# Kernel optimization log

Hardware: AMD Instinct MI355X
Metric: run time of the kernel (lower is better)

## Reference

```python
import jax, jax.numpy as jnp
import numpy as np

N, E = 20000, 320000
IN, HID, R, HEADS = 128, 256, 4, 4
C = HID // HEADS  # per-head dim


def setup_inputs() -> dict:
    key = jax.random.key(0)
    ks = jax.random.split(key, 20)
    g = lambda k, s, sc=0.05: jax.random.normal(k, s, jnp.float32) * sc
    return {
        'x': g(ks[0], (N, IN), 1.0),
        'edge_index': jax.random.randint(ks[1], (2, E), 0, N),
        'edge_type': jax.random.randint(ks[2], (E,), 0, R),
        'h_prev': g(ks[3], (N, HID), 1.0),
        # RGCN layer 1: relation weights, root weight, bias
        'W1': g(ks[4], (R, IN, HID)), 'root1': g(ks[5], (IN, HID)), 'b1': jnp.zeros((HID,), jnp.float32),
        # RGCN layer 2
        'W2': g(ks[6], (R, HID, HID)), 'root2': g(ks[7], (HID, HID)), 'b2': jnp.zeros((HID,), jnp.float32),
        # TransformerConv linears (query/key/value/skip), each Linear(HID, HEADS*C)
        'Wq': g(ks[8], (HID, HID)), 'bq': jnp.zeros((HID,), jnp.float32),
        'Wk': g(ks[9], (HID, HID)), 'bk': jnp.zeros((HID,), jnp.float32),
        'Wv': g(ks[10], (HID, HID)), 'bv': jnp.zeros((HID,), jnp.float32),
        'Wskip': g(ks[11], (HID, HID)), 'bskip': jnp.zeros((HID,), jnp.float32),
        # GRUCell (torch layout: [3*HID, in], gates ordered r, z, n)
        'W_ih': g(ks[12], (3 * HID, HID)), 'b_ih': jnp.zeros((3 * HID,), jnp.float32),
        'W_hh': g(ks[13], (3 * HID, HID)), 'b_hh': jnp.zeros((3 * HID,), jnp.float32),
    }


def rgcn(x, src, dst, etype, W, Wroot, b):
    # PyG RGCNConv: out_i = x_i @ Wroot + b + sum_r mean_{j in N_r(i)} x_j @ W_r
    n = x.shape[0]
    out = x @ Wroot + b
    xs = x[src]  # [E, F_in]
    for r in range(W.shape[0]):  # small fixed relation count
        mask = (etype == r).astype(x.dtype)  # [E]
        msg = (xs @ W[r]) * mask[:, None]  # [E, F_out]
        agg = jax.ops.segment_sum(msg, dst, num_segments=n)
        cnt = jax.ops.segment_sum(mask, dst, num_segments=n)
        out = out + agg / jnp.maximum(cnt, 1.0)[:, None]
    return out


def transformer_conv(x, src, dst, Wq, bq, Wk, bk, Wv, bv, Wskip, bskip):
    # PyG TransformerConv, concat=True, root_weight=True
    n = x.shape[0]
    q = (x @ Wq + bq).reshape(n, HEADS, C)
    k = (x @ Wk + bk).reshape(n, HEADS, C)
    v = (x @ Wv + bv).reshape(n, HEADS, C)
    score = jnp.einsum('ehc,ehc->eh', q[dst], k[src]) * (1.0 / np.sqrt(C))  # [E, H]
    smax = jax.ops.segment_max(score, dst, num_segments=n)  # [N, H]
    ex = jnp.exp(score - smax[dst])
    denom = jax.ops.segment_sum(ex, dst, num_segments=n)
    alpha = ex / jnp.maximum(denom[dst], 1e-16)  # edge softmax per dst node
    out = jax.ops.segment_sum(alpha[:, :, None] * v[src], dst, num_segments=n)  # [N, H, C]
    return out.reshape(n, HEADS * C) + x @ Wskip + bskip


def gru_cell(xi, h, W_ih, b_ih, W_hh, b_hh):
    gi = xi @ W_ih.T + b_ih
    gh = h @ W_hh.T + b_hh
    ir, iz, inn = jnp.split(gi, 3, axis=1)
    hr, hz, hn = jnp.split(gh, 3, axis=1)
    r = jax.nn.sigmoid(ir + hr)
    z = jax.nn.sigmoid(iz + hz)
    nw = jnp.tanh(inn + r * hn)
    return (1.0 - z) * nw + z * h


def reference(x, edge_index, edge_type, h_prev, W1, root1, b1, W2, root2, b2,
              Wq, bq, Wk, bk, Wv, bv, Wskip, bskip, W_ih, b_ih, W_hh, b_hh):
    src, dst = edge_index[0], edge_index[1]
    h = jax.nn.relu(rgcn(x, src, dst, edge_type, W1, root1, b1))
    h = jax.nn.relu(rgcn(h, src, dst, edge_type, W2, root2, b2))
    h = transformer_conv(h, src, dst, Wq, bq, Wk, bk, Wv, bv, Wskip, bskip)
    h = gru_cell(h, h_prev, W_ih, b_ih, W_hh, b_hh)
    return h
```

## Files before the change

kernel.cpp:

```cpp
#include <hip/hip_runtime.h>
#include <hip/hip_bf16.h>
#include <stdint.h>

#define N_NODES 20000
#define E_EDGES 320000
#define IN_F    128
#define HIDF    256
#define R_REL   4
#define NRKEYS  (N_NODES*R_REL)
#define SCAN_BLOCKS 80

typedef __attribute__((ext_vector_type(8))) short  short8;
typedef __attribute__((ext_vector_type(4))) float  floatx4;

__device__ __forceinline__ float bf2f(__hip_bfloat16 v){ return __bfloat162float(v); }
__device__ __forceinline__ __hip_bfloat16 f2bf(float v){ return __float2bfloat16(v); }
__device__ __forceinline__ float bfbits2f(unsigned short u){ return __uint_as_float(((unsigned)u)<<16); }
__device__ __forceinline__ unsigned short f2bfbits(float v){
    __hip_bfloat16 h = __float2bfloat16(v);
    return *(unsigned short*)&h;
}
__device__ __forceinline__ unsigned pack_bf2(float a, float b){
    return (unsigned)f2bfbits(a) | ((unsigned)f2bfbits(b) << 16);
}

__device__ __forceinline__ void gload_lds16(const void* g, void* l)
{
    __builtin_amdgcn_global_load_lds((const __attribute__((address_space(1))) void*)g,
                                     (__attribute__((address_space(3))) void*)l, 16, 0, 0);
}

template<int N>
__device__ __forceinline__ void wait_vm()
{
    if constexpr (N == 0)      asm volatile("s_waitcnt vmcnt(0)" ::: "memory");
    else if constexpr (N == 3) asm volatile("s_waitcnt vmcnt(3)" ::: "memory");
    else if constexpr (N == 4) asm volatile("s_waitcnt vmcnt(4)" ::: "memory");
    else                       asm volatile("s_waitcnt vmcnt(0)" ::: "memory");
}

__device__ __forceinline__ int2 xcd_swizzle()
{
    int gx = gridDim.x, gy = gridDim.y;
    int nwg = gx * gy;
    int lin = blockIdx.x + gx * blockIdx.y;
    int q = nwg >> 3, r = nwg & 7;
    int k = lin & 7, i = lin >> 3;
    int j = (k < r ? k*(q+1) : r*(q+1) + (k-r)*q) + i;
    return make_int2(j / gy, j % gy);
}

__global__ void count_kernel(const int* __restrict__ ei, const int* __restrict__ et,
                             int* __restrict__ cnt)
{
    int e = blockIdx.x*256 + threadIdx.x;
    if (e >= E_EDGES) return;
    int dst = ei[E_EDGES + e];
    atomicAdd(&cnt[dst*R_REL + et[e]], 1);
}

__global__ __launch_bounds__(1024) void scan_reduce_kernel(const int* __restrict__ cnt,
                                                           int* __restrict__ blocksum)
{
    int ix = blockIdx.x*1024 + threadIdx.x;
    int v = (ix < NRKEYS) ? cnt[ix] : 0;
    #pragma unroll
    for (int o=32;o>0;o>>=1) v += __shfl_xor(v, o, 64);
    __shared__ int wsum[16];
    int wave = threadIdx.x >> 6, lane = threadIdx.x & 63;
    if (lane == 0) wsum[wave] = v;
    __syncthreads();
    if (threadIdx.x == 0) {
        int s = 0;
        #pragma unroll
        for (int w=0;w<16;w++) s += wsum[w];
        blocksum[blockIdx.x] = s;
    }
}

__global__ __launch_bounds__(128) void scan_sums_kernel(const int* __restrict__ blocksum,
                                                        int* __restrict__ blockoff)
{
    __shared__ int s[128];
    int t = threadIdx.x;
    int v = (t < SCAN_BLOCKS) ? blocksum[t] : 0;
    s[t] = v; __syncthreads();
    for (int off=1; off<128; off<<=1) {
        int u = (t>=off) ? s[t-off] : 0;
        __syncthreads();
        s[t] += u;
        __syncthreads();
    }
    if (t < SCAN_BLOCKS) blockoff[t] = s[t] - v;
}

__global__ __launch_bounds__(1024) void scan_apply_kernel(const int* __restrict__ cnt,
                                                          const int* __restrict__ blockoff,
                                                          int* __restrict__ row_ptr,
                                                          int* __restrict__ cursor)
{
    __shared__ int s[1024];
    int t = threadIdx.x;
    int ix = blockIdx.x*1024 + t;
    int v = (ix < NRKEYS) ? cnt[ix] : 0;
    s[t] = v; __syncthreads();
    for (int off=1; off<1024; off<<=1) {
        int u = (t>=off) ? s[t-off] : 0;
        __syncthreads();
        s[t] += u;
        __syncthreads();
    }
    if (ix < NRKEYS) {
        int excl = blockoff[blockIdx.x] + s[t] - v;
        row_ptr[ix] = excl;
        cursor[ix]  = excl;
        if (ix == NRKEYS-1) row_ptr[NRKEYS] = excl + v;
    }
}

__global__ void fill_kernel(const int* __restrict__ ei, const int* __restrict__ et,
                            int* __restrict__ cursor, int* __restrict__ csr_src)
{
    int e = blockIdx.x*256 + threadIdx.x;
    if (e >= E_EDGES) return;
    int src = ei[e];
    int dst = ei[E_EDGES + e];
    int key = dst*R_REL + et[e];
    int pos = atomicAdd(&cursor[key], 1);
    csr_src[pos] = src;
}

__global__ void make_b1t(const float* __restrict__ root1,
                         const float* __restrict__ W1,
                         __hip_bfloat16* __restrict__ B1t)
{
    int idx = blockIdx.x*256 + threadIdx.x;
    if (idx >= 256*640) return;
    int n = idx / 640, k = idx % 640;
    float v;
    if (k < 128) v = root1[k*256 + n];
    else         v = W1[(k-128)*256 + n];
    B1t[idx] = f2bf(v);
}

__global__ void make_b2t(const float* __restrict__ root2,
                         const float* __restrict__ W2,
                         __hip_bfloat16* __restrict__ B2t)
{
    int idx = blockIdx.x*256 + threadIdx.x;
    if (idx >= 256*1280) return;
    int n = idx / 1280, k = idx % 1280;
    float v;
    if (k < 256) v = root2[k*256 + n];
    else         v = W2[(k-256)*256 + n];
    B2t[idx] = f2bf(v);
}

__global__ void make_b3t(const float* __restrict__ Wq, const float* __restrict__ Wk,
                         const float* __restrict__ Wv, const float* __restrict__ Wsk,
                         const float* __restrict__ bq, const float* __restrict__ bk,
                         const float* __restrict__ bv, const float* __restrict__ bsk,
                         __hip_bfloat16* __restrict__ B3t, float* __restrict__ bias3)
{
    int idx = blockIdx.x*256 + threadIdx.x;
    if (idx >= 1024*256) return;
    int n = idx / 256, k = idx % 256;
    int g = n >> 8, nn = n & 255;
    const float* W = (g==0)?Wq:(g==1)?Wk:(g==2)?Wv:Wsk;
    B3t[idx] = f2bf(W[k*256 + nn]);
    if (k == 0) {
        const float* B = (g==0)?bq:(g==1)?bk:(g==2)?bv:bsk;
        bias3[n] = B[nn];
    }
}

__global__ void cvt_f32_bf16(const float* __restrict__ in, __hip_bfloat16* __restrict__ out, int n)
{
    int i = blockIdx.x*256 + threadIdx.x;
    if (i < n) out[i] = f2bf(in[i]);
}

__global__ __launch_bounds__(256) void agg1_kernel(const float* __restrict__ x,
                                                   const int* __restrict__ row_ptr,
                                                   const int* __restrict__ csr_src,
                                                   __hip_bfloat16* __restrict__ A1)
{
    int b = blockIdx.x*4 + (threadIdx.x >> 6);
    int lane = threadIdx.x & 63;
    int i = b >> 2, r = b & 3;
    int e0 = row_ptr[b], e1 = row_ptr[b+1];
    float sx0=0.f,sy0=0.f, sx1=0.f,sy1=0.f, sx2=0.f,sy2=0.f, sx3=0.f,sy3=0.f;
    int e = e0;
    for (; e+4 <= e1; e += 4) {
        int i0=csr_src[e], i1=csr_src[e+1], i2=csr_src[e+2], i3=csr_src[e+3];
        float2 v0 = *(const float2*)(x + (size_t)i0*IN_F + lane*2);
        float2 v1 = *(const float2*)(x + (size_t)i1*IN_F + lane*2);
        float2 v2 = *(const float2*)(x + (size_t)i2*IN_F + lane*2);
        float2 v3 = *(const float2*)(x + (size_t)i3*IN_F + lane*2);
        sx0+=v0.x; sy0+=v0.y; sx1+=v1.x; sy1+=v1.y;
        sx2+=v2.x; sy2+=v2.y; sx3+=v3.x; sy3+=v3.y;
    }
    for (; e < e1; e++) {
        int i0 = csr_src[e];
        float2 v = *(const float2*)(x + (size_t)i0*IN_F + lane*2);
        sx0+=v.x; sy0+=v.y;
    }
    float sx = (sx0+sx1)+(sx2+sx3);
    float sy = (sy0+sy1)+(sy2+sy3);
    float inv = (e1>e0) ? 1.f/(float)(e1-e0) : 0.f;
    *(unsigned*)(A1 + (size_t)i*640 + 128 + r*128 + lane*2) = pack_bf2(sx*inv, sy*inv);
    if (r == 0) {
        float2 v = *(const float2*)(x + (size_t)i*IN_F + lane*2);
        *(unsigned*)(A1 + (size_t)i*640 + lane*2) = pack_bf2(v.x, v.y);
    }
}

__global__ __launch_bounds__(256) void agg2_kernel(const int* __restrict__ row_ptr,
                                                   const int* __restrict__ csr_src,
                                                   __hip_bfloat16* __restrict__ A2)
{
    int b = blockIdx.x*4 + (threadIdx.x >> 6);
    int lane = threadIdx.x & 63;
    int i = b >> 2, r = b & 3;
    int e0 = row_ptr[b], e1 = row_ptr[b+1];
    float a0=0.f,a1=0.f,a2=0.f,a3=0.f;
    float b0=0.f,b1=0.f,b2=0.f,b3=0.f;
    float c0=0.f,c1=0.f,c2=0.f,c3=0.f;
    float d0=0.f,d1=0.f,d2=0.f,d3=0.f;
    int e = e0;
    for (; e+4 <= e1; e += 4) {
        int i0=csr_src[e], i1=csr_src[e+1], i2=csr_src[e+2], i3=csr_src[e+3];
        ushort4 u0 = *(const ushort4*)(A2 + (size_t)i0*1280 + lane*4);
        ushort4 u1 = *(const ushort4*)(A2 + (size_t)i1*1280 + lane*4);
        ushort4 u2 = *(const ushort4*)(A2 + (size_t)i2*1280 + lane*4);
        ushort4 u3 = *(const ushort4*)(A2 + (size_t)i3*1280 + lane*4);
        a0+=bfbits2f(u0.x); a1+=bfbits2f(u0.y); a2+=bfbits2f(u0.z); a3+=bfbits2f(u0.w);
        b0+=bfbits2f(u1.x); b1+=bfbits2f(u1.y); b2+=bfbits2f(u1.z); b3+=bfbits2f(u1.w);
        c0+=bfbits2f(u2.x); c1+=bfbits2f(u2.y); c2+=bfbits2f(u2.z); c3+=bfbits2f(u2.w);
        d0+=bfbits2f(u3.x); d1+=bfbits2f(u3.y); d2+=bfbits2f(u3.z); d3+=bfbits2f(u3.w);
    }
    for (; e < e1; e++) {
        int i0 = csr_src[e];
        ushort4 u = *(const ushort4*)(A2 + (size_t)i0*1280 + lane*4);
        a0+=bfbits2f(u.x); a1+=bfbits2f(u.y); a2+=bfbits2f(u.z); a3+=bfbits2f(u.w);
    }
    float s0=(a0+b0)+(c0+d0), s1=(a1+b1)+(c1+d1), s2=(a2+b2)+(c2+d2), s3=(a3+b3)+(c3+d3);
    float inv = (e1>e0) ? 1.f/(float)(e1-e0) : 0.f;
    uint2 w;
    w.x = pack_bf2(s0*inv, s1*inv);
    w.y = pack_bf2(s2*inv, s3*inv);
    *(uint2*)(A2 + (size_t)i*1280 + 256 + r*256 + lane*4) = w;
}

template<int MI>
__device__ __forceinline__ void gemm_bt_body(const __hip_bfloat16* __restrict__ A, int lda,
                                             const __hip_bfloat16* __restrict__ Bt,
                                             const float* __restrict__ bias,
                                             __hip_bfloat16* __restrict__ C, int ldc,
                                             int M, int K, int relu,
                                             int tile_m, int tile_n,
                                             __hip_bfloat16* lds_a, __hip_bfloat16* lds_b)
{
    constexpr int A_ELEMS = MI*1024;
    constexpr int B_ELEMS = 4096;
    constexpr int L = MI/2 + 2;
    const int tid  = threadIdx.x;
    const int wave = tid >> 6;
    const int lane = tid & 63;
    const int wm = wave >> 1, wn = wave & 1;
    const int fm = lane & 15;
    const int q  = lane >> 4;
    const int sw = (q ^ ((fm >> 1) & 3)) * 8;

    floatx4 acc[MI][4];
    #pragma unroll
    for (int i=0;i<MI;i++)
        #pragma unroll
        for (int j=0;j<4;j++) acc[i][j] = (floatx4){0.f,0.f,0.f,0.f};

    const int srow   = lane >> 2;
    const int schunk = lane & 3;
    size_t a_goff[MI/2];
    #pragma unroll
    for (int s = 0; s < MI/2; ++s) {
        int r = (s*4 + wave)*16 + srow;
        int c = schunk ^ ((r >> 1) & 3);
        a_goff[s] = (size_t)min(tile_m + r, M-1)*lda + c*8;
    }
    size_t b_goff[2];
    #pragma unroll
    for (int s = 0; s < 2; ++s) {
        int r = (s*4 + wave)*16 + srow;
        int c = schunk ^ ((r >> 1) & 3);
        b_goff[s] = (size_t)(tile_n + r)*K + c*8;
    }

    const int nt = K >> 5;

    auto issue = [&](int t, int bufi) {
        const int kn = t << 5;
        #pragma unroll
        for (int s = 0; s < MI/2; ++s)
            gload_lds16(A + a_goff[s] + kn, lds_a + bufi*A_ELEMS + (s*4 + wave)*512);
        #pragma unroll
        for (int s = 0; s < 2; ++s)
            gload_lds16(Bt + b_goff[s] + kn, lds_b + bufi*B_ELEMS + (s*4 + wave)*512);
    };

    issue(0, 0);
    if (nt > 1) { issue(1, 1); wait_vm<L>(); }
    else        { wait_vm<0>(); }
    __builtin_amdgcn_s_barrier();

    int cur = 0, nx2 = 2;
    for (int t = 0; t < nt; ++t) {
        if (t + 2 < nt) issue(t + 2, nx2);

        const __hip_bfloat16* la = lds_a + cur*A_ELEMS;
        const __hip_bfloat16* lb = lds_b + cur*B_ELEMS;
        short8 afr[MI], bfr[4];
        #pragma unroll
        for (int i=0;i<MI;i++)
            afr[i] = *(const short8*)(la + (wm*(MI*16) + i*16 + fm)*32 + sw);
        #pragma unroll
        for (int j=0;j<4;j++)
            bfr[j] = *(const short8*)(lb + (wn*64 + j*16 + fm)*32 + sw);

        __builtin_amdgcn_s_setprio(1);
        #pragma unroll
        for (int i=0;i<MI;i++)
            #pragma unroll
            for (int j=0;j<4;j++)
                acc[i][j] = __builtin_amdgcn_mfma_f32_16x16x32_bf16(afr[i], bfr[j], acc[i][j], 0,0,0);
        __builtin_amdgcn_s_setprio(0);

        if (t + 1 < nt) {
            if (t + 2 < nt) wait_vm<L>();
            else            wait_vm<0>();
            __builtin_amdgcn_s_barrier();
            cur = (cur == 2) ? 0 : cur + 1;
            nx2 = (nx2 == 2) ? 0 : nx2 + 1;
        }
    }

    const int crow_base = tile_m + wm*(MI*16);
    const int ccol_base = tile_n + wn*64;
    #pragma unroll
    for (int i=0;i<MI;i++) {
        #pragma unroll
        for (int j=0;j<4;j++) {
            int c  = ccol_base + j*16 + fm;
            float bb = bias[c];
            #pragma unroll
            for (int rg=0; rg<4; rg++) {
                int r = crow_base + i*16 + q*4 + rg;
                if (r < M) {
                    float v = acc[i][j][rg] + bb;
                    if (relu) v = fmaxf(v, 0.f);
                    C[(size_t)r*ldc + c] = f2bf(v);
                }
            }
        }
    }
}

template<int MI>
__global__ __launch_bounds__(256) void gemm_bt_t(const __hip_bfloat16* __restrict__ A, int lda,
                                                 const __hip_bfloat16* __restrict__ Bt,
                                                 const float* __restrict__ bias,
                                                 __hip_bfloat16* __restrict__ C, int ldc,
                                                 int M, int K, int relu)
{
    __shared__ __align__(16) __hip_bfloat16 lds_a[3*MI*1024];
    __shared__ __align__(16) __hip_bfloat16 lds_b[3*4096];
    int2 xy = xcd_swizzle();
    gemm_bt_body<MI>(A, lda, Bt, bias, C, ldc, M, K, relu,
                     xy.x*(MI*32), xy.y*128, lds_a, lds_b);
}

__global__ __launch_bounds__(256) void gemm_bt_dual(const __hip_bfloat16* __restrict__ A0,
                                                    const __hip_bfloat16* __restrict__ A1,
                                                    const __hip_bfloat16* __restrict__ Bt0,
                                                    const __hip_bfloat16* __restrict__ Bt1,
                                                    const float* __restrict__ bias0,
                                                    const float* __restrict__ bias1,
                                                    __hip_bfloat16* __restrict__ C0,
                                                    __hip_bfloat16* __restrict__ C1)
{
    __shared__ __align__(16) __hip_bfloat16 lds_a[3*4096];
    __shared__ __align__(16) __hip_bfloat16 lds_b[3*4096];
    int2 xy = xcd_swizzle();
    int which = xy.y >= 6;
    int ty    = which ? (xy.y - 6) : xy.y;
    gemm_bt_body<4>(which ? A1 : A0, 256,
                    which ? Bt1 : Bt0,
                    which ? bias1 : bias0,
                    which ? C1 : C0, 768,
                    N_NODES, 256, 0,
                    xy.x*128, ty*128, lds_a, lds_b);
}

__global__ __launch_bounds__(256) void score_kernel(const __hip_bfloat16* __restrict__ qkvs,
                                                    const int* __restrict__ row_ptr,
                                                    const int* __restrict__ csr_src,
                                                    float* __restrict__ score)
{
    int i = blockIdx.x*4 + (threadIdx.x >> 6);
    int lane = threadIdx.x & 63;
    int h = lane >> 4, d4 = lane & 15;
    int e0 = row_ptr[i*R_REL], e1 = row_ptr[i*R_REL + R_REL];
    ushort4 qv = *(const ushort4*)(qkvs + (size_t)i*1024 + lane*4);
    float qx=bfbits2f(qv.x), qy=bfbits2f(qv.y), qz=bfbits2f(qv.z), qw=bfbits2f(qv.w);
    float* sp = score + (size_t)h*E_EDGES;
    int j = e0;
    for (; j+2 <= e1; j += 2) {
        int s0 = csr_src[j], s1 = csr_src[j+1];
        ushort4 k0 = *(const ushort4*)(qkvs + (size_t)s0*1024 + 256 + lane*4);
        ushort4 k1 = *(const ushort4*)(qkvs + (size_t)s1*1024 + 256 + lane*4);
        float d0 = qx*bfbits2f(k0.x)+qy*bfbits2f(k0.y)+qz*bfbits2f(k0.z)+qw*bfbits2f(k0.w);
        float d1 = qx*bfbits2f(k1.x)+qy*bfbits2f(k1.y)+qz*bfbits2f(k1.z)+qw*bfbits2f(k1.w);
        #pragma unroll
        for (int o=1;o<16;o<<=1){ d0 += __shfl_xor(d0,o,64); d1 += __shfl_xor(d1,o,64); }
        if (d4 == 0) { sp[j] = d0*0.125f; sp[j+1] = d1*0.125f; }
    }
    for (; j < e1; j++) {
        int s0 = csr_src[j];
        ushort4 k0 = *(const ushort4*)(qkvs + (size_t)s0*1024 + 256 + lane*4);
        float d0 = qx*bfbits2f(k0.x)+qy*bfbits2f(k0.y)+qz*bfbits2f(k0.z)+qw*bfbits2f(k0.w);
        #pragma unroll
        for (int o=1;o<16;o<<=1) d0 += __shfl_xor(d0,o,64);
        if (d4 == 0) sp[j] = d0*0.125f;
    }
}

__global__ __launch_bounds__(256) void attn_agg_kernel(const __hip_bfloat16* __restrict__ qkvs,
                                                       const float* __restrict__ score,
                                                       const int* __restrict__ row_ptr,
                                                       const int* __restrict__ csr_src,
                                                       __hip_bfloat16* __restrict__ hatt)
{
    int i = blockIdx.x*4 + (threadIdx.x >> 6);
    int lane = threadIdx.x & 63;
    int h  = lane >> 4;
    int d4 = lane & 15;
    int e0 = row_ptr[i*R_REL], e1 = row_ptr[i*R_REL + R_REL];
    int deg = e1 - e0;
    const float* sp = score + (size_t)h*E_EDGES + e0;

    float m = -1e30f;
    for (int j = d4; j < deg; j += 16) m = fmaxf(m, sp[j]);
    #pragma unroll
    for (int o=1;o<16;o<<=1) m = fmaxf(m, __shfl_xor(m, o, 64));

    float ssum = 0.f;
    for (int j = d4; j < deg; j += 16) ssum += __expf(sp[j] - m);
    #pragma unroll
    for (int o=1;o<16;o<<=1) ssum += __shfl_xor(ssum, o, 64);
    float inv = 1.f / fmaxf(ssum, 1e-16f);

    float ax=0.f, ay=0.f, az=0.f, aw=0.f;
    int j = 0;
    for (; j+4 <= deg; j += 4) {
        int s0=csr_src[e0+j], s1=csr_src[e0+j+1], s2=csr_src[e0+j+2], s3=csr_src[e0+j+3];
        float w0 = __expf(sp[j]   - m) * inv;
        float w1 = __expf(sp[j+1] - m) * inv;
        float w2 = __expf(sp[j+2] - m) * inv;
        float w3 = __expf(sp[j+3] - m) * inv;
        ushort4 u0 = *(const ushort4*)(qkvs + (size_t)s0*1024 + 512 + lane*4);
        ushort4 u1 = *(const ushort4*)(qkvs + (size_t)s1*1024 + 512 + lane*4);
        ushort4 u2 = *(const ushort4*)(qkvs + (size_t)s2*1024 + 512 + lane*4);
        ushort4 u3 = *(const ushort4*)(qkvs + (size_t)s3*1024 + 512 + lane*4);
        ax += w0*bfbits2f(u0.x) + w1*bfbits2f(u1.x) + w2*bfbits2f(u2.x) + w3*bfbits2f(u3.x);
        ay += w0*bfbits2f(u0.y) + w1*bfbits2f(u1.y) + w2*bfbits2f(u2.y) + w3*bfbits2f(u3.y);
        az += w0*bfbits2f(u0.z) + w1*bfbits2f(u1.z) + w2*bfbits2f(u2.z) + w3*bfbits2f(u3.z);
        aw += w0*bfbits2f(u0.w) + w1*bfbits2f(u1.w) + w2*bfbits2f(u2.w) + w3*bfbits2f(u3.w);
    }
    for (; j < deg; j++) {
        int s = csr_src[e0+j];
        float w = __expf(sp[j] - m) * inv;
        ushort4 u = *(const ushort4*)(qkvs + (size_t)s*1024 + 512 + lane*4);
        ax += w*bfbits2f(u.x); ay += w*bfbits2f(u.y);
        az += w*bfbits2f(u.z); aw += w*bfbits2f(u.w);
    }
    ushort4 sk = *(const ushort4*)(qkvs + (size_t)i*1024 + 768 + lane*4);
    uint2 w;
    w.x = pack_bf2(ax + bfbits2f(sk.x), ay + bfbits2f(sk.y));
    w.y = pack_bf2(az + bfbits2f(sk.z), aw + bfbits2f(sk.w));
    *(uint2*)(hatt + (size_t)i*256 + lane*4) = w;
}

__global__ void gru_kernel(const __hip_bfloat16* __restrict__ gi,
                           const __hip_bfloat16* __restrict__ gh,
                           const float* __restrict__ hprev,
                           float* __restrict__ out)
{
    int idx = blockIdx.x*256 + threadIdx.x;
    if (idx >= N_NODES*HIDF) return;
    int i = idx / HIDF, c = idx % HIDF;
    size_t gb = (size_t)i*768;
    float ir = bf2f(gi[gb + c]), iz = bf2f(gi[gb + 256 + c]), in = bf2f(gi[gb + 512 + c]);
    float hr = bf2f(gh[gb + c]), hz = bf2f(gh[gb + 256 + c]), hn = bf2f(gh[gb + 512 + c]);
    float r = 1.f/(1.f + __expf(-(ir+hr)));
    float z = 1.f/(1.f + __expf(-(iz+hz)));
    float n = tanhf(in + r*hn);
    float h = hprev[idx];
    out[idx] = (1.f - z)*n + z*h;
}

extern "C" void kernel_launch(void* const* d_in, const int* in_sizes, int n_in,
                              void* d_out, int out_size, void* d_ws, size_t ws_size,
                              hipStream_t stream)
{
    const float* x       = (const float*)d_in[0];
    const int* edge_index= (const int*)d_in[1];
    const int* edge_type = (const int*)d_in[2];
    const float* hprev   = (const float*)d_in[3];
    const float* W1      = (const float*)d_in[4];
    const float* root1   = (const float*)d_in[5];
    const float* b1      = (const float*)d_in[6];
    const float* W2      = (const float*)d_in[7];
    const float* root2   = (const float*)d_in[8];
    const float* b2      = (const float*)d_in[9];
    const float* Wq      = (const float*)d_in[10];
    const float* bq      = (const float*)d_in[11];
    const float* Wk      = (const float*)d_in[12];
    const float* bk      = (const float*)d_in[13];
    const float* Wv      = (const float*)d_in[14];
    const float* bv      = (const float*)d_in[15];
    const float* Wskip   = (const float*)d_in[16];
    const float* bskip   = (const float*)d_in[17];
    const float* W_ih    = (const float*)d_in[18];
    const float* b_ih    = (const float*)d_in[19];
    const float* W_hh    = (const float*)d_in[20];
    const float* b_hh    = (const float*)d_in[21];

    char* ws = (char*)d_ws;
    size_t off = 0;
    auto take = [&](size_t bytes)->char* {
        char* p = ws + off;
        off = (off + bytes + 255) & ~(size_t)255;
        return p;
    };
    int* cnt        = (int*)take((size_t)NRKEYS*4);
    int* row_ptr    = (int*)take((size_t)(NRKEYS+1)*4);
    int* cursor     = (int*)take((size_t)NRKEYS*4);
    int* csr_src    = (int*)take((size_t)E_EDGES*4);
    int* blocksum   = (int*)take((size_t)SCAN_BLOCKS*4);
    int* blockoff   = (int*)take((size_t)(SCAN_BLOCKS+1)*4);
    float* score    = (float*)take((size_t)R_REL*E_EDGES*4);
    __hip_bfloat16* B1t   = (__hip_bfloat16*)take((size_t)256*640*2);
    __hip_bfloat16* B2t   = (__hip_bfloat16*)take((size_t)256*1280*2);
    __hip_bfloat16* B3t   = (__hip_bfloat16*)take((size_t)1024*256*2);
    __hip_bfloat16* Biht  = (__hip_bfloat16*)take((size_t)768*256*2);
    __hip_bfloat16* Bhht  = (__hip_bfloat16*)take((size_t)768*256*2);
    float*          bias3 = (float*)take((size_t)1024*4);
    __hip_bfloat16* hprev_bf = (__hip_bfloat16*)take((size_t)N_NODES*256*2);
    char* P1 = take((size_t)N_NODES*640*2);
    char* P2 = take((size_t)N_NODES*1536*2);

    __hip_bfloat16* A1   = (__hip_bfloat16*)P1;
    __hip_bfloat16* h2   = (__hip_bfloat16*)P1;
    __hip_bfloat16* hatt = (__hip_bfloat16*)P1;
    __hip_bfloat16* A2   = (__hip_bfloat16*)P2;
    __hip_bfloat16* qkvs = (__hip_bfloat16*)P2;
    __hip_bfloat16* gi   = (__hip_bfloat16*)P2;
    __hip_bfloat16* gh   = (__hip_bfloat16*)(P2 + (size_t)N_NODES*768*2);

    hipMemsetAsync(cnt, 0, (size_t)NRKEYS*4, stream);
    count_kernel<<<(E_EDGES+255)/256, 256, 0, stream>>>(edge_index, edge_type, cnt);
    scan_reduce_kernel<<<SCAN_BLOCKS, 1024, 0, stream>>>(cnt, blocksum);
    scan_sums_kernel<<<1, 128, 0, stream>>>(blocksum, blockoff);
    scan_apply_kernel<<<SCAN_BLOCKS, 1024, 0, stream>>>(cnt, blockoff, row_ptr, cursor);
    fill_kernel<<<(E_EDGES+255)/256, 256, 0, stream>>>(edge_index, edge_type, cursor, csr_src);

    make_b1t<<<(256*640+255)/256, 256, 0, stream>>>(root1, W1, B1t);
    make_b2t<<<(256*1280+255)/256, 256, 0, stream>>>(root2, W2, B2t);
    make_b3t<<<(1024*256+255)/256, 256, 0, stream>>>(Wq, Wk, Wv, Wskip, bq, bk, bv, bskip, B3t, bias3);
    cvt_f32_bf16<<<(768*256+255)/256, 256, 0, stream>>>(W_ih, Biht, 768*256);
    cvt_f32_bf16<<<(768*256+255)/256, 256, 0, stream>>>(W_hh, Bhht, 768*256);
    cvt_f32_bf16<<<(N_NODES*256+255)/256, 256, 0, stream>>>(hprev, hprev_bf, N_NODES*256);

    agg1_kernel<<<NRKEYS/4, 256, 0, stream>>>(x, row_ptr, csr_src, A1);

    dim3 g12(313, 2);
    gemm_bt_t<2><<<g12, 256, 0, stream>>>(A1, 640, B1t, b1, A2, 1280, N_NODES, 640, 1);

    agg2_kernel<<<NRKEYS/4, 256, 0, stream>>>(row_ptr, csr_src, A2);

    gemm_bt_t<2><<<g12, 256, 0, stream>>>(A2, 1280, B2t, b2, h2, 256, N_NODES, 1280, 1);

    dim3 g3(157, 8);
    gemm_bt_t<4><<<g3, 256, 0, stream>>>(h2, 256, B3t, bias3, qkvs, 1024, N_NODES, 256, 0);

    score_kernel<<<N_NODES/4, 256, 0, stream>>>(qkvs, row_ptr, csr_src, score);
    attn_agg_kernel<<<N_NODES/4, 256, 0, stream>>>(qkvs, score, row_ptr, csr_src, hatt);

    dim3 g45(157, 12);
    gemm_bt_dual<<<g45, 256, 0, stream>>>(hatt, hprev_bf, Biht, Bhht, b_ih, b_hh, gi, gh);

    gru_kernel<<<(N_NODES*HIDF+255)/256, 256, 0, stream>>>(gi, gh, hprev, (float*)d_out);
}
```

Measured before the change: 434.1 us.

## Replace LDS-tiled K=256 GEMMs with per-wave direct-load MFMA kernels

The QKV/skip projection GEMM and the dual GRU input/hidden GEMMs (both K=256) move from the LDS triple-buffered tiled body to a new body. In the new body each wave loads its A and B fragments straight from global memory and computes a 64x64 output tile with 16 accumulators. This removes LDS staging and barriers and uses smaller block tiles (64x256), giving more blocks. The cost is that the four waves in a block no longer share A through LDS, so A is re-read from global/L2 per wave. The epilogue also writes scattered bf16 elements without coalescing.

```diff
diff --git a/kernel.cpp b/kernel.cpp
--- a/kernel.cpp
+++ b/kernel.cpp
@@ -378,26 +378,88 @@
                      xy.x*(MI*32), xy.y*128, lds_a, lds_b);
 }
 
-__global__ __launch_bounds__(256) void gemm_bt_dual(const __hip_bfloat16* __restrict__ A0,
-                                                    const __hip_bfloat16* __restrict__ A1,
-                                                    const __hip_bfloat16* __restrict__ Bt0,
-                                                    const __hip_bfloat16* __restrict__ Bt1,
-                                                    const float* __restrict__ bias0,
-                                                    const float* __restrict__ bias1,
-                                                    __hip_bfloat16* __restrict__ C0,
-                                                    __hip_bfloat16* __restrict__ C1)
-{
-    __shared__ __align__(16) __hip_bfloat16 lds_a[3*4096];
-    __shared__ __align__(16) __hip_bfloat16 lds_b[3*4096];
+__device__ __forceinline__ void gemm_wave_body(const __hip_bfloat16* __restrict__ A,
+                                               const __hip_bfloat16* __restrict__ Bt,
+                                               const float* __restrict__ bias,
+                                               __hip_bfloat16* __restrict__ C, int ldc,
+                                               int M, int tile_m, int tile_n)
+{
+    const int lane = threadIdx.x & 63;
+    const int fm = lane & 15;
+    const int q  = lane >> 4;
+
+    floatx4 acc[4][4];
+    #pragma unroll
+    for (int i=0;i<4;i++)
+        #pragma unroll
+        for (int j=0;j<4;j++) acc[i][j] = (floatx4){0.f,0.f,0.f,0.f};
+
+    const __hip_bfloat16* ap[4];
+    const __hip_bfloat16* bp[4];
+    #pragma unroll
+    for (int i=0;i<4;i++)
+        ap[i] = A + (size_t)min(tile_m + i*16 + fm, M-1)*256 + q*8;
+    #pragma unroll
+    for (int j=0;j<4;j++)
+        bp[j] = Bt + (size_t)(tile_n + j*16 + fm)*256 + q*8;
+
+    #pragma unroll
+    for (int t = 0; t < 8; ++t) {
+        short8 av[4], bv[4];
+        #pragma unroll
+        for (int i=0;i<4;i++) av[i] = *(const short8*)(ap[i] + t*32);
+        #pragma unroll
+        for (int j=0;j<4;j++) bv[j] = *(const short8*)(bp[j] + t*32);
+        #pragma unroll
+        for (int i=0;i<4;i++)
+            #pragma unroll
+            for (int j=0;j<4;j++)
+                acc[i][j] = __builtin_amdgcn_mfma_f32_16x16x32_bf16(av[i], bv[j], acc[i][j], 0,0,0);
+    }
+
+    #pragma unroll
+    for (int i=0;i<4;i++) {
+        #pragma unroll
+        for (int j=0;j<4;j++) {
+            int c  = tile_n + j*16 + fm;
+            float bb = bias[c];
+            #pragma unroll
+            for (int rg=0; rg<4; rg++) {
+                int r = tile_m + i*16 + q*4 + rg;
+                if (r < M) C[(size_t)r*ldc + c] = f2bf(acc[i][j][rg] + bb);
+            }
+        }
+    }
+}
+
+__global__ __launch_bounds__(256) void gemm_wave_single(const __hip_bfloat16* __restrict__ A,
+                                                        const __hip_bfloat16* __restrict__ Bt,
+                                                        const float* __restrict__ bias,
+                                                        __hip_bfloat16* __restrict__ C, int ldc)
+{
     int2 xy = xcd_swizzle();
-    int which = xy.y >= 6;
-    int ty    = which ? (xy.y - 6) : xy.y;
-    gemm_bt_body<4>(which ? A1 : A0, 256,
-                    which ? Bt1 : Bt0,
-                    which ? bias1 : bias0,
-                    which ? C1 : C0, 768,
-                    N_NODES, 256, 0,
-                    xy.x*128, ty*128, lds_a, lds_b);
+    int wave = threadIdx.x >> 6;
+    gemm_wave_body(A, Bt, bias, C, ldc, N_NODES, xy.x*64, xy.y*256 + wave*64);
+}
+
+__global__ __launch_bounds__(256) void gemm_wave_dual(const __hip_bfloat16* __restrict__ A0,
+                                                      const __hip_bfloat16* __restrict__ A1,
+                                                      const __hip_bfloat16* __restrict__ Bt0,
+                                                      const __hip_bfloat16* __restrict__ Bt1,
+                                                      const float* __restrict__ bias0,
+                                                      const float* __restrict__ bias1,
+                                                      __hip_bfloat16* __restrict__ C0,
+                                                      __hip_bfloat16* __restrict__ C1)
+{
+    int2 xy = xcd_swizzle();
+    int wave = threadIdx.x >> 6;
+    int which = xy.y >= 3;
+    int ny    = which ? (xy.y - 3) : xy.y;
+    gemm_wave_body(which ? A1 : A0,
+                   which ? Bt1 : Bt0,
+                   which ? bias1 : bias0,
+                   which ? C1 : C0, 768,
+                   N_NODES, xy.x*64, ny*256 + wave*64);
 }
 
 __global__ __launch_bounds__(256) void score_kernel(const __hip_bfloat16* __restrict__ qkvs,
@@ -589,14 +651,12 @@
 
     gemm_bt_t<2><<<g12, 256, 0, stream>>>(A2, 1280, B2t, b2, h2, 256, N_NODES, 1280, 1);
 
-    dim3 g3(157, 8);
-    gemm_bt_t<4><<<g3, 256, 0, stream>>>(h2, 256, B3t, bias3, qkvs, 1024, N_NODES, 256, 0);
+    gemm_wave_single<<<dim3(313, 4), 256, 0, stream>>>(h2, B3t, bias3, qkvs, 1024);
 
     score_kernel<<<N_NODES/4, 256, 0, stream>>>(qkvs, row_ptr, csr_src, score);
     attn_agg_kernel<<<N_NODES/4, 256, 0, stream>>>(qkvs, score, row_ptr, csr_src, hatt);
 
-    dim3 g45(157, 12);
-    gemm_bt_dual<<<g45, 256, 0, stream>>>(hatt, hprev_bf, Biht, Bhht, b_ih, b_hh, gi, gh);
+    gemm_wave_dual<<<dim3(313, 6), 256, 0, stream>>>(hatt, hprev_bf, Biht, Bhht, b_ih, b_hh, gi, gh);
 
     gru_kernel<<<(N_NODES*HIDF+255)/256, 256, 0, stream>>>(gi, gh, hprev, (float*)d_out);
 }
```

After: 487.4 us. 1.12x slower.

## Fuse GRU gate GEMMs with the GRU elementwise epilogue in one kernel

Applied to the files above, without the earlier changes.

Replaces the dual GEMM that wrote the bf16 gi/gh buffers, and the separate GRU elementwise kernel, with one kernel. Each block computes a 64-row by 32-column tile for all three gates of both the input and hidden GEMMs, using a new triple-buffered LDS pipeline, then applies the GRU nonlinearity and writes the fp32 output directly. This drops the write and reread of two N×768 intermediates and one kernel launch. In exchange, the tiles are smaller and the gate-interleaved tiling is new, so MFMA efficiency may drop and the B tiles are reloaded across more blocks.

```diff
diff --git a/kernel.cpp b/kernel.cpp
--- a/kernel.cpp
+++ b/kernel.cpp
@@ -36,6 +36,7 @@
     if constexpr (N == 0)      asm volatile("s_waitcnt vmcnt(0)" ::: "memory");
     else if constexpr (N == 3) asm volatile("s_waitcnt vmcnt(3)" ::: "memory");
     else if constexpr (N == 4) asm volatile("s_waitcnt vmcnt(4)" ::: "memory");
+    else if constexpr (N == 5) asm volatile("s_waitcnt vmcnt(5)" ::: "memory");
     else                       asm volatile("s_waitcnt vmcnt(0)" ::: "memory");
 }
 
@@ -378,26 +379,128 @@
                      xy.x*(MI*32), xy.y*128, lds_a, lds_b);
 }
 
-__global__ __launch_bounds__(256) void gemm_bt_dual(const __hip_bfloat16* __restrict__ A0,
-                                                    const __hip_bfloat16* __restrict__ A1,
-                                                    const __hip_bfloat16* __restrict__ Bt0,
-                                                    const __hip_bfloat16* __restrict__ Bt1,
-                                                    const float* __restrict__ bias0,
-                                                    const float* __restrict__ bias1,
-                                                    __hip_bfloat16* __restrict__ C0,
-                                                    __hip_bfloat16* __restrict__ C1)
-{
-    __shared__ __align__(16) __hip_bfloat16 lds_a[3*4096];
-    __shared__ __align__(16) __hip_bfloat16 lds_b[3*4096];
+__global__ __launch_bounds__(256) void gemm_gru_fused(
+    const __hip_bfloat16* __restrict__ A0,
+    const __hip_bfloat16* __restrict__ A1,
+    const __hip_bfloat16* __restrict__ Bt0,
+    const __hip_bfloat16* __restrict__ Bt1,
+    const float* __restrict__ b_ih, const float* __restrict__ b_hh,
+    const float* __restrict__ hprev, float* __restrict__ out)
+{
+    constexpr int BUF_ELEMS = 10240;
+    __shared__ __align__(16) __hip_bfloat16 lds[3*BUF_ELEMS];
     int2 xy = xcd_swizzle();
-    int which = xy.y >= 6;
-    int ty    = which ? (xy.y - 6) : xy.y;
-    gemm_bt_body<4>(which ? A1 : A0, 256,
-                    which ? Bt1 : Bt0,
-                    which ? bias1 : bias0,
-                    which ? C1 : C0, 768,
-                    N_NODES, 256, 0,
-                    xy.x*128, ty*128, lds_a, lds_b);
+    const int tile_m = xy.x * 64;
+    const int c0     = xy.y * 32;
+    const int tid = threadIdx.x, wave = tid >> 6, lane = tid & 63;
+    const int fm = lane & 15, q = lane >> 4;
+    const int sw = (q ^ ((fm >> 1) & 3)) * 8;
+
+    const int sub = lane >> 2, ch = lane & 3;
+    const __hip_bfloat16* gsrc[5];
+    int dstoff[5];
+    #pragma unroll
+    for (int s = 0; s < 5; ++s) {
+        int seg = wave*5 + s;
+        if (seg < 8) {
+            int fr = seg*16 + sub;
+            int mat = fr >> 6, rl = fr & 63;
+            int c = ch ^ ((fr >> 1) & 3);
+            int grow = min(tile_m + rl, N_NODES-1);
+            gsrc[s] = (mat ? A1 : A0) + (size_t)grow*256 + c*8;
+            dstoff[s] = seg*512;
+        } else {
+            int fs = seg - 8;
+            int fr = fs*16 + sub;
+            int grp = fr >> 5, ri = fr & 31;
+            int mat = grp >= 3, gate = mat ? grp-3 : grp;
+            int c = ch ^ ((fr >> 1) & 3);
+            int grow = gate*256 + c0 + ri;
+            gsrc[s] = (mat ? Bt1 : Bt0) + (size_t)grow*256 + c*8;
+            dstoff[s] = 4096 + fs*512;
+        }
+    }
+
+    floatx4 acc[2][3][2];
+    #pragma unroll
+    for (int m=0;m<2;m++)
+        #pragma unroll
+        for (int g=0;g<3;g++)
+            #pragma unroll
+            for (int f=0;f<2;f++) acc[m][g][f] = (floatx4){0.f,0.f,0.f,0.f};
+
+    auto issue = [&](int t, int bufi) {
+        const int kn = t << 5;
+        #pragma unroll
+        for (int s = 0; s < 5; ++s)
+            gload_lds16(gsrc[s] + kn, lds + bufi*BUF_ELEMS + dstoff[s]);
+    };
+
+    issue(0, 0);
+    issue(1, 1);
+    wait_vm<5>();
+    __builtin_amdgcn_s_barrier();
+
+    int cur = 0, nx2 = 2;
+    #pragma unroll 1
+    for (int t = 0; t < 8; ++t) {
+        if (t + 2 < 8) issue(t + 2, nx2);
+
+        const __hip_bfloat16* lb = lds + cur*BUF_ELEMS;
+        short8 af[2], bf_[2][3][2];
+        #pragma unroll
+        for (int m=0;m<2;m++)
+            af[m] = *(const short8*)(lb + (m*64 + wave*16 + fm)*32 + sw);
+        #pragma unroll
+        for (int m=0;m<2;m++)
+            #pragma unroll
+            for (int g=0;g<3;g++)
+                #pragma unroll
+                for (int f=0;f<2;f++)
+                    bf_[m][g][f] = *(const short8*)(lb + 4096 + (((m*3+g)*32) + f*16 + fm)*32 + sw);
+
+        __builtin_amdgcn_s_setprio(1);
+        #pragma unroll
+        for (int m=0;m<2;m++)
+            #pragma unroll
+            for (int g=0;g<3;g++)
+                #pragma unroll
+                for (int f=0;f<2;f++)
+                    acc[m][g][f] = __builtin_amdgcn_mfma_f32_16x16x32_bf16(af[m], bf_[m][g][f], acc[m][g][f], 0,0,0);
+        __builtin_amdgcn_s_setprio(0);
+
+        if (t + 1 < 8) {
+            if (t + 2 < 8) wait_vm<5>();
+            else           wait_vm<0>();
+            __builtin_amdgcn_s_barrier();
+            cur = (cur == 2) ? 0 : cur + 1;
+            nx2 = (nx2 == 2) ? 0 : nx2 + 1;
+        }
+    }
+
+    #pragma unroll
+    for (int f=0; f<2; ++f) {
+        int c = c0 + f*16 + fm;
+        float bir = b_ih[c], biz = b_ih[256+c], bin = b_ih[512+c];
+        float bhr = b_hh[c], bhz = b_hh[256+c], bhn = b_hh[512+c];
+        #pragma unroll
+        for (int rg=0; rg<4; ++rg) {
+            int r = tile_m + wave*16 + q*4 + rg;
+            if (r < N_NODES) {
+                float gir = acc[0][0][f][rg] + bir;
+                float giz = acc[0][1][f][rg] + biz;
+                float gin = acc[0][2][f][rg] + bin;
+                float ghr = acc[1][0][f][rg] + bhr;
+                float ghz = acc[1][1][f][rg] + bhz;
+                float ghn = acc[1][2][f][rg] + bhn;
+                float rr = 1.f/(1.f + __expf(-(gir + ghr)));
+                float zz = 1.f/(1.f + __expf(-(giz + ghz)));
+                float nn = tanhf(gin + rr*ghn);
+                float h  = hprev[(size_t)r*256 + c];
+                out[(size_t)r*256 + c] = (1.f - zz)*nn + zz*h;
+            }
+        }
+    }
 }
 
 __global__ __launch_bounds__(256) void score_kernel(const __hip_bfloat16* __restrict__ qkvs,
@@ -487,24 +590,6 @@
     w.x = pack_bf2(ax + bfbits2f(sk.x), ay + bfbits2f(sk.y));
     w.y = pack_bf2(az + bfbits2f(sk.z), aw + bfbits2f(sk.w));
     *(uint2*)(hatt + (size_t)i*256 + lane*4) = w;
-}
-
-__global__ void gru_kernel(const __hip_bfloat16* __restrict__ gi,
-                           const __hip_bfloat16* __restrict__ gh,
-                           const float* __restrict__ hprev,
-                           float* __restrict__ out)
-{
-    int idx = blockIdx.x*256 + threadIdx.x;
-    if (idx >= N_NODES*HIDF) return;
-    int i = idx / HIDF, c = idx % HIDF;
-    size_t gb = (size_t)i*768;
-    float ir = bf2f(gi[gb + c]), iz = bf2f(gi[gb + 256 + c]), in = bf2f(gi[gb + 512 + c]);
-    float hr = bf2f(gh[gb + c]), hz = bf2f(gh[gb + 256 + c]), hn = bf2f(gh[gb + 512 + c]);
-    float r = 1.f/(1.f + __expf(-(ir+hr)));
-    float z = 1.f/(1.f + __expf(-(iz+hz)));
-    float n = tanhf(in + r*hn);
-    float h = hprev[idx];
-    out[idx] = (1.f - z)*n + z*h;
 }
 
 extern "C" void kernel_launch(void* const* d_in, const int* in_sizes, int n_in,
@@ -563,8 +648,6 @@
     __hip_bfloat16* hatt = (__hip_bfloat16*)P1;
     __hip_bfloat16* A2   = (__hip_bfloat16*)P2;
     __hip_bfloat16* qkvs = (__hip_bfloat16*)P2;
-    __hip_bfloat16* gi   = (__hip_bfloat16*)P2;
-    __hip_bfloat16* gh   = (__hip_bfloat16*)(P2 + (size_t)N_NODES*768*2);
 
     hipMemsetAsync(cnt, 0, (size_t)NRKEYS*4, stream);
     count_kernel<<<(E_EDGES+255)/256, 256, 0, stream>>>(edge_index, edge_type, cnt);
@@ -595,8 +678,6 @@
     score_kernel<<<N_NODES/4, 256, 0, stream>>>(qkvs, row_ptr, csr_src, score);
     attn_agg_kernel<<<N_NODES/4, 256, 0, stream>>>(qkvs, score, row_ptr, csr_src, hatt);
 
-    dim3 g45(157, 12);
-    gemm_bt_dual<<<g45, 256, 0, stream>>>(hatt, hprev_bf, Biht, Bhht, b_ih, b_hh, gi, gh);
-
-    gru_kernel<<<(N_NODES*HIDF+255)/256, 256, 0, stream>>>(gi, gh, hprev, (float*)d_out);
-}
+    gemm_gru_fused<<<dim3(313, 8), 256, 0, stream>>>(hatt, hprev_bf, Biht, Bhht,
+                                                     b_ih, b_hh, hprev, (float*)d_out);
+}
```

New measurement: 431.2 us. Within noise of the previous version (-0.7%).
